# Kernel tuning notes

Hardware: AMD Instinct MI355X
Metric: run time of the kernel (lower is better)

Reference implementation:

```python
import jax, jax.numpy as jnp
import numpy as np

NUM_EMBEDDINGS = 8192
EMBEDDING_DIM = 256
BETA = 0.25


def setup_inputs() -> dict:
    key = jax.random.key(0)
    k1, k2 = jax.random.split(key)
    z = jax.random.normal(k1, (16, 256, 32, 32), dtype=jnp.float32)
    # torch init: uniform(-1/K, 1/K)
    emb_w = jax.random.uniform(k2, (NUM_EMBEDDINGS, EMBEDDING_DIM),
                               dtype=jnp.float32,
                               minval=-1.0 / NUM_EMBEDDINGS,
                               maxval=1.0 / NUM_EMBEDDINGS)
    return {"z": z, "emb_w": emb_w}


def reference(z, emb_w):
    B, C, H, W = z.shape
    z_bhwc = jnp.transpose(z, (0, 2, 3, 1))          # [B,H,W,C]
    flat = z_bhwc.reshape(-1, C)                      # [N,C]
    d = (jnp.sum(flat * flat, axis=1, keepdims=True)
         + jnp.sum(emb_w * emb_w, axis=1)
         - 2.0 * flat @ emb_w.T)                      # [N,K]
    idx = jnp.argmin(d, axis=1)                       # [N]
    # direct gather (mathematically identical to one-hot @ emb_w)
    quantized = emb_w[idx].reshape(z_bhwc.shape)      # [B,H,W,C]
    q_latent_loss = jnp.mean((jax.lax.stop_gradient(quantized) - z_bhwc) ** 2)
    e_latent_loss = jnp.mean((quantized - jax.lax.stop_gradient(z_bhwc)) ** 2)
    loss = q_latent_loss + BETA * e_latent_loss
    # straight-through estimator
    quantized_st = z_bhwc + jax.lax.stop_gradient(quantized - z_bhwc)
    out = jnp.transpose(quantized_st, (0, 3, 1, 2))   # [B,C,H,W]
    return out, loss, idx.reshape(B, -1)
```

## Files before the change

### kernel.cpp

```cpp
#include <hip/hip_runtime.h>
#include <cstdint>
#include <cstddef>

#define N_PIX   16384
#define K_EMB   8192
#define DDIM    256

#define WS_A8       0
#define WS_E8       4194304
#define WS_KEYS     6291456
#define WS_ZSQ      23068672
#define WS_ESQ      23134208
#define WS_LOSS     23166976
#define WS_CNT      23166984

typedef float f32x4 __attribute__((ext_vector_type(4)));

__device__ __forceinline__ unsigned int f32_sortable(float f) {
    unsigned int u = __float_as_uint(f);
    return (u & 0x80000000u) ? ~u : (u | 0x80000000u);
}

__device__ __forceinline__ unsigned char f2fp8(float x) {
    unsigned ub = __float_as_uint(x);
    unsigned sgn = (ub >> 24) & 0x80u;
    unsigned b = ub & 0x7FFFFFFFu;
    unsigned out;
    if (__uint_as_float(b) < 0.015625f) {
        out = (unsigned)(int)rintf(__uint_as_float(b) * 512.0f);
    } else {
        unsigned r = b + 0x7FFFFu + ((b >> 20) & 1u);
        int er = (int)(r >> 23) - 127;
        out = (unsigned)(((er + 7) << 3) | ((r >> 20) & 7u));
    }
    return (unsigned char)(out | sgn);
}

#if defined(__has_builtin)
#if __has_builtin(__builtin_amdgcn_cvt_pk_fp8_f32)
#define HAVE_CVT_FP8 1
#endif
#endif

__device__ __forceinline__ unsigned pack4_fp8(float a, float b, float c, float d) {
#ifdef HAVE_CVT_FP8
    int pk = 0;
    pk = __builtin_amdgcn_cvt_pk_fp8_f32(a, b, pk, false);
    pk = __builtin_amdgcn_cvt_pk_fp8_f32(c, d, pk, true);
    return (unsigned)pk;
#else
    return (unsigned)f2fp8(a) | ((unsigned)f2fp8(b) << 8)
         | ((unsigned)f2fp8(c) << 16) | ((unsigned)f2fp8(d) << 24);
#endif
}

__device__ __forceinline__ void async16(const unsigned char* g, unsigned char* l) {
    __builtin_amdgcn_global_load_lds(
        (const __attribute__((address_space(1))) void*)g,
        (__attribute__((address_space(3))) void*)l, 16, 0, 0);
}

__device__ __forceinline__ float np_pairwise_sq256(const float* row) {
    float r[16];
#pragma unroll
    for (int j = 0; j < 16; ++j) r[j] = 0.f;
#pragma unroll
    for (int c = 0; c < 256; ++c) {
        float x  = row[c];
        float sq = __fmul_rn(x, x);
        int slot = ((c >> 7) << 3) | (c & 7);
        r[slot] = __fadd_rn(r[slot], sq);
    }
    float h0 = __fadd_rn(
        __fadd_rn(__fadd_rn(r[0], r[1]), __fadd_rn(r[2], r[3])),
        __fadd_rn(__fadd_rn(r[4], r[5]), __fadd_rn(r[6], r[7])));
    float h1 = __fadd_rn(
        __fadd_rn(__fadd_rn(r[8], r[9]), __fadd_rn(r[10], r[11])),
        __fadd_rn(__fadd_rn(r[12], r[13]), __fadd_rn(r[14], r[15])));
    return __fadd_rn(h0, h1);
}

__device__ __forceinline__ size_t cm_addr(int r, int c) {
    int ks = c >> 5;
    int h  = (c >> 4) & 1;
    int s  = h ^ ((r >> 2) & 1);
    return (size_t)ks * 4096 + (size_t)r * 32 + s * 16 + (c & 15);
}

__global__ __launch_bounds__(256) void prep_kernel(
        const float* __restrict__ z, const float* __restrict__ emb,
        unsigned char* __restrict__ Af8, unsigned char* __restrict__ Ef8,
        float* __restrict__ zsq, float* __restrict__ esq,
        double* __restrict__ lossAcc, unsigned* __restrict__ doneCnt) {
    __shared__ float tile[32][257];
    int blk = blockIdx.x;
    int t   = threadIdx.x;
    if (blk < 512) {
        int b   = blk >> 5;
        int hw0 = (blk & 31) * 32;
        const float* zb = z + (size_t)b * 262144 + hw0;
        int px = t & 31;
        int cb = t >> 5;
#pragma unroll
        for (int cc = 0; cc < 32; ++cc) {
            int c = cc * 8 + cb;
            tile[px][c] = zb[(size_t)c * 1024 + px];
        }
        __syncthreads();
        int p0 = b * 1024 + hw0;
        int wv = t >> 6, lane = t & 63;
#pragma unroll
        for (int iter = 0; iter < 8; ++iter) {
            int pl = iter * 4 + wv;
            unsigned pk = pack4_fp8(tile[pl][lane * 4 + 0], tile[pl][lane * 4 + 1],
                                    tile[pl][lane * 4 + 2], tile[pl][lane * 4 + 3]);
            int p  = p0 + pl;
            int mb = p >> 7, r = p & 127;
            *(unsigned*)(Af8 + (size_t)mb * 32768 + cm_addr(r, lane * 4)) = pk;
        }
        if (t < 32) zsq[p0 + t] = np_pairwise_sq256(tile[t]);
        if (blk == 0 && t == 0) { *lossAcc = 0.0; *doneCnt = 0u; }
    } else {
        int k0 = (blk - 512) * 32;
        const float4* eg = (const float4*)(emb + (size_t)k0 * DDIM);
#pragma unroll
        for (int i = 0; i < 8; ++i) {
            int idx = i * 256 + t;
            int row = idx >> 6, c4 = idx & 63;
            float4 v = eg[idx];
            *(float4*)&tile[row][c4 * 4] = v;
        }
        __syncthreads();
#pragma unroll
        for (int i = 0; i < 8; ++i) {
            int idx = i * 256 + t;
            int row = idx >> 6, c4 = idx & 63;
            const float* rp = &tile[row][c4 * 4];
            int kg = k0 + row;
            int nb = kg >> 7, rr = kg & 127;
            *(unsigned*)(Ef8 + (size_t)nb * 32768 + cm_addr(rr, c4 * 4)) =
                pack4_fp8(rp[0] * 8192.0f, rp[1] * 8192.0f,
                          rp[2] * 8192.0f, rp[3] * 8192.0f);
        }
        if (t < 32) esq[k0 + t] = np_pairwise_sq256(tile[t]);
    }
}

__device__ __forceinline__ unsigned pack_key(float w) {
    float uf = __builtin_fmaf(w, -512.0f, 262144.0f);
    uf = fminf(uf, 524287.0f);
    unsigned u = (unsigned)uf;
    return (u << 13) | (__float_as_uint(w) & 0x1FFFu);
}

__global__ __launch_bounds__(256) void mfma_score_kernel(
        const unsigned char* __restrict__ Af8,
        const unsigned char* __restrict__ Ef8,
        unsigned int* __restrict__ keys) {
    union SM {
        struct { unsigned char As[8][4096]; unsigned char Bs[8][4096]; } k;
        struct { uint2 ep[128][33]; } e;
    };
    __shared__ SM sm;

    const int g  = blockIdx.x;
    const int mb = blockIdx.y;
    const int t = threadIdx.x;
    const int w = t >> 6, lane = t & 63;
    const int wm = w >> 1, wn = w & 1;
    const int quad = lane >> 4, l16 = lane & 15;

    const unsigned char* Ag = Af8 + (size_t)mb * 32768 + t * 16;
#pragma unroll
    for (int ks = 0; ks < 8; ++ks)
        async16(Ag + ks * 4096, &sm.k.As[ks][t * 16]);
    {
        const unsigned char* Eg = Ef8 + (size_t)(g * 4) * 32768 + t * 16;
#pragma unroll
        for (int ks = 0; ks < 8; ++ks)
            async16(Eg + ks * 4096, &sm.k.Bs[ks][t * 16]);
    }

    int aaddr[4], baddr[4];
#pragma unroll
    for (int fi = 0; fi < 4; ++fi) {
        int row = wm * 64 + fi * 16 + l16;
        int gg  = (quad >> 1) ^ ((row >> 2) & 1);
        aaddr[fi] = row * 32 + gg * 16 + (quad & 1) * 8;
    }
#pragma unroll
    for (int fj = 0; fj < 4; ++fj) {
        int row = wn * 64 + fj * 16 + l16;
        int gg  = (quad >> 1) ^ ((row >> 2) & 1);
        baddr[fj] = row * 32 + gg * 16 + (quad & 1) * 8;
    }

    __syncthreads();

    long long afr[4][8];
#pragma unroll
    for (int fi = 0; fi < 4; ++fi)
#pragma unroll
        for (int ks = 0; ks < 8; ++ks)
            afr[fi][ks] = *(const long long*)&sm.k.As[ks][aaddr[fi]];

    const float NEGINF = __int_as_float(0xFF800000);
    float t2a[16], t2b[16];
#pragma unroll
    for (int i = 0; i < 16; ++i) { t2a[i] = NEGINF; t2b[i] = NEGINF; }

#pragma unroll 1
    for (int j = 0; j < 4; ++j) {
        f32x4 acc[4][4];
#pragma unroll
        for (int i = 0; i < 4; ++i)
#pragma unroll
            for (int jj = 0; jj < 4; ++jj)
#pragma unroll
                for (int r = 0; r < 4; ++r) acc[i][jj][r] = 0.f;

#pragma unroll
        for (int ks = 0; ks < 8; ++ks) {
            long long bfr[4];
#pragma unroll
            for (int fj = 0; fj < 4; ++fj)
                bfr[fj] = *(const long long*)&sm.k.Bs[ks][baddr[fj]];
            __builtin_amdgcn_s_setprio(1);
#pragma unroll
            for (int fi = 0; fi < 4; ++fi)
#pragma unroll
                for (int fj = 0; fj < 4; ++fj)
                    acc[fi][fj] = __builtin_amdgcn_mfma_f32_16x16x32_fp8_fp8(
                        afr[fi][ks], bfr[fj], acc[fi][fj], 0, 0, 0);
            __builtin_amdgcn_s_setprio(0);
        }
        __syncthreads();

        if (j < 3) {
            const unsigned char* Eg =
                Ef8 + (size_t)(g * 4 + j + 1) * 32768 + t * 16;
#pragma unroll
            for (int ks = 0; ks < 8; ++ks)
                async16(Eg + ks * 4096, &sm.k.Bs[ks][t * 16]);
        }

        const int nb = g * 4 + j;
        const unsigned idx0 = (unsigned)(nb * 128 + wn * 64 + l16);
#pragma unroll
        for (int fi = 0; fi < 4; ++fi) {
#pragma unroll
            for (int r = 0; r < 4; ++r) {
                const int ai = fi * 4 + r;
                float a0 = t2a[ai], b0 = t2b[ai];
#pragma unroll
                for (int fj = 0; fj < 4; ++fj) {
                    float v = acc[fi][fj][r];
                    float wv = __uint_as_float(
                        (__float_as_uint(v) & 0xFFFFE000u) | (idx0 + fj * 16));
                    float mn = fminf(a0, wv);
                    a0 = fmaxf(a0, wv);
                    b0 = fmaxf(b0, mn);
                }
                t2a[ai] = a0; t2b[ai] = b0;
            }
        }
        __syncthreads();
    }

#pragma unroll
    for (int fi = 0; fi < 4; ++fi) {
#pragma unroll
        for (int r = 0; r < 4; ++r) {
            const int ai = fi * 4 + r;
            int row = wm * 64 + fi * 16 + quad * 4 + r;
            sm.e.ep[row][wn * 16 + l16] =
                make_uint2(pack_key(t2a[ai]), pack_key(t2b[ai]));
        }
    }
    __syncthreads();

    {
        int row = t >> 1, half = t & 1, h0 = half * 16;
        uint2 mv = sm.e.ep[row][h0];
#pragma unroll
        for (int i = 1; i < 16; ++i) {
            uint2 av = sm.e.ep[row][h0 + i];
            unsigned n0 = min(mv.x, av.x);
            unsigned n1 = min(max(mv.x, av.x), min(mv.y, av.y));
            mv.x = n0; mv.y = n1;
        }
        ((uint2*)keys)[(size_t)(g * 2 + half) * N_PIX + (mb * 128 + row)] = mv;
    }
}

__global__ __launch_bounds__(256) void final_kernel(
        const unsigned int* __restrict__ keys,
        const float* __restrict__ z, const float* __restrict__ emb,
        const float* __restrict__ zsq, const float* __restrict__ esq,
        float* __restrict__ out, float* __restrict__ idx_out,
        float* __restrict__ loss_out,
        double* __restrict__ lossAcc, unsigned* __restrict__ doneCnt) {
    __shared__ float ztile[16][260];
    __shared__ uint2 kt[16][33];
    __shared__ int sidx[16];
    int blk = blockIdx.x;
    int b = blk >> 6, hh = blk & 63;
    int t = threadIdx.x;
    int p0 = b * 1024 + hh * 16;
    const float* zb = z + (size_t)b * 262144 + hh * 16;
    {
        int px = t & 15, cb = t >> 4;
#pragma unroll
        for (int cc = 0; cc < 16; ++cc) {
            int c = cc * 16 + cb;
            ztile[px][c] = zb[(size_t)c * 1024 + px];
        }
    }
    {
        const uint2* kg = (const uint2*)keys;
#pragma unroll
        for (int itr = 0; itr < 2; ++itr) {
            int idx = itr * 256 + t;
            int px = idx & 15, hf = idx >> 4;
            kt[px][hf] = kg[(size_t)hf * N_PIX + p0 + px];
        }
    }
    __syncthreads();

    int wq = t >> 6, lane = t & 63;
#pragma unroll 1
    for (int i = 0; i < 4; ++i) {
        int px = wq * 4 + i;
        int p  = p0 + px;
        uint2 ka = (lane < 32) ? kt[px][lane] : make_uint2(~0u, ~0u);
        unsigned m = min(ka.x, ka.y);
#pragma unroll
        for (int off = 32; off >= 1; off >>= 1)
            m = min(m, (unsigned)__shfl_xor((int)m, off, 64));
        unsigned thr = (m >> 13) + 1600;

        float4 zv = *(const float4*)&ztile[px][lane * 4];
        float zs = zsq[p];
        unsigned long long best = ~0ull;
#pragma unroll 1
        for (int pass = 0; pass < 2; ++pass) {
            unsigned kv = (pass == 0) ? ka.x : ka.y;
            unsigned long long mm = __ballot((kv >> 13) <= thr);
            while (mm) {
                int src = (int)__builtin_ctzll(mm);
                mm &= mm - 1;
                unsigned keyv = (unsigned)__shfl((int)kv, src, 64);
                int k = (int)(keyv & 0x1FFFu);
                const float4 ev = *(const float4*)(emb + (size_t)k * DDIM + lane * 4);
                double d = (double)zv.x * ev.x + (double)zv.y * ev.y
                         + (double)zv.z * ev.z + (double)zv.w * ev.w;
#pragma unroll
                for (int off = 32; off >= 1; off >>= 1)
                    d += __shfl_down(d, off, 64);
                d = __shfl(d, 0, 64);
                float df = (float)d;
                float s  = __fsub_rn(__fadd_rn(zs, esq[k]), __fmul_rn(2.0f, df));
                unsigned long long key =
                    ((unsigned long long)f32_sortable(s) << 32) | (unsigned)k;
                best = key < best ? key : best;
            }
        }
        if (lane == 0) {
            int k = (int)(unsigned)(best & 0xffffffffu);
            sidx[px] = k;
            idx_out[p] = (float)k;
        }
    }
    __syncthreads();

    int px2 = t & 15, cy = t >> 4;
    int kk = sidx[px2];
    const float* er = emb + (size_t)kk * DDIM;
    float* ob = out + (size_t)b * 262144 + hh * 16;
    float local = 0.f;
#pragma unroll 4
    for (int it = 0; it < 16; ++it) {
        int c = it * 16 + cy;
        float q = er[c];
        float d = q - ztile[px2][c];
        ob[(size_t)c * 1024 + px2] = q;
        local += d * d;
    }
#pragma unroll
    for (int off = 32; off >= 1; off >>= 1) local += __shfl_down(local, off, 64);
    __shared__ float wsum[4];
    if ((t & 63) == 0) wsum[t >> 6] = local;
    __syncthreads();
    if (t == 0) {
        double s = (double)wsum[0] + (double)wsum[1]
                 + (double)wsum[2] + (double)wsum[3];
        atomicAdd(lossAcc, s);
        __threadfence();
        unsigned old = atomicAdd(doneCnt, 1u);
        if (old == 1023u) {
            double tot = atomicAdd(lossAcc, 0.0);
            *loss_out = (float)(tot * (1.25 / 4194304.0));
        }
    }
}

extern "C" void kernel_launch(void* const* d_in, const int* in_sizes, int n_in,
                              void* d_out, int out_size, void* d_ws, size_t ws_size,
                              hipStream_t stream) {
    const float* z   = (const float*)d_in[0];
    const float* emb = (const float*)d_in[1];
    float* out = (float*)d_out;
    char* ws = (char*)d_ws;

    unsigned char* Af8 = (unsigned char*)(ws + WS_A8);
    unsigned char* Ef8 = (unsigned char*)(ws + WS_E8);
    unsigned int* keys = (unsigned int*)(ws + WS_KEYS);
    float* zsq      = (float*)(ws + WS_ZSQ);
    float* esq      = (float*)(ws + WS_ESQ);
    double* lossAcc = (double*)(ws + WS_LOSS);
    unsigned* doneCnt = (unsigned*)(ws + WS_CNT);

    prep_kernel<<<768, 256, 0, stream>>>(z, emb, Af8, Ef8, zsq, esq,
                                         lossAcc, doneCnt);
    mfma_score_kernel<<<dim3(16, 128), 256, 0, stream>>>(Af8, Ef8, keys);
    final_kernel<<<1024, 256, 0, stream>>>(keys, z, emb, zsq, esq,
                                           out, out + 4194305, out + 4194304,
                                           lossAcc, doneCnt);
}
```

Before: 197.9 us.

## Compact rerank candidates into shared list and score them with 16-lane groups

The final kernel's exact-distance rerank is restructured. Candidate codes for each of the 16 pixels are first compacted into shared memory with a prefix-sum offset table. They are then scored in double precision by 16-lane groups over a flat candidate list, and the best key per pixel is found by a grouped min reduction. Previously one wave processed each candidate serially with a 64-lane shuffle reduction. This is meant to balance uneven candidate counts across waves and shorten reductions, at the cost of extra shared memory, barriers and a binary search per candidate. The prep kernel's z tile load also now uses float4 global reads.

```diff
diff --git a/kernel.cpp b/kernel.cpp
--- a/kernel.cpp
+++ b/kernel.cpp
@@ -99,12 +99,16 @@
         int b   = blk >> 5;
         int hw0 = (blk & 31) * 32;
         const float* zb = z + (size_t)b * 262144 + hw0;
-        int px = t & 31;
-        int cb = t >> 5;
-#pragma unroll
-        for (int cc = 0; cc < 32; ++cc) {
-            int c = cc * 8 + cb;
-            tile[px][c] = zb[(size_t)c * 1024 + px];
+        int c0  = t >> 3;
+        int px4 = t & 7;
+#pragma unroll
+        for (int cc = 0; cc < 8; ++cc) {
+            int c = cc * 32 + c0;
+            float4 v = *(const float4*)&zb[(size_t)c * 1024 + px4 * 4];
+            tile[px4 * 4 + 0][c] = v.x;
+            tile[px4 * 4 + 1][c] = v.y;
+            tile[px4 * 4 + 2][c] = v.z;
+            tile[px4 * 4 + 3][c] = v.w;
         }
         __syncthreads();
         int p0 = b * 1024 + hw0;
@@ -302,7 +306,14 @@
         double* __restrict__ lossAcc, unsigned* __restrict__ doneCnt) {
     __shared__ float ztile[16][260];
     __shared__ uint2 kt[16][33];
-    __shared__ int sidx[16];
+    __shared__ int   scand[16][64];
+    __shared__ unsigned long long ckey[1024];
+    __shared__ int   soff[17];
+    __shared__ int   scnt[16];
+    __shared__ int   pxmap[1024];
+    __shared__ float szs[16];
+    __shared__ int   sidx[16];
+
     int blk = blockIdx.x;
     int b = blk >> 6, hh = blk & 63;
     int t = threadIdx.x;
@@ -325,50 +336,102 @@
             kt[px][hf] = kg[(size_t)hf * N_PIX + p0 + px];
         }
     }
-    __syncthreads();
-
-    int wq = t >> 6, lane = t & 63;
+    if (t < 16) szs[t] = zsq[p0 + t];
+    __syncthreads();
+
+    {
+        int wq = t >> 6, lane = t & 63;
 #pragma unroll 1
-    for (int i = 0; i < 4; ++i) {
-        int px = wq * 4 + i;
-        int p  = p0 + px;
-        uint2 ka = (lane < 32) ? kt[px][lane] : make_uint2(~0u, ~0u);
-        unsigned m = min(ka.x, ka.y);
-#pragma unroll
-        for (int off = 32; off >= 1; off >>= 1)
-            m = min(m, (unsigned)__shfl_xor((int)m, off, 64));
-        unsigned thr = (m >> 13) + 1600;
-
-        float4 zv = *(const float4*)&ztile[px][lane * 4];
-        float zs = zsq[p];
+        for (int i = 0; i < 4; ++i) {
+            int px = wq * 4 + i;
+            uint2 ka = (lane < 32) ? kt[px][lane] : make_uint2(~0u, ~0u);
+            unsigned m = min(ka.x, ka.y);
+#pragma unroll
+            for (int off = 32; off >= 1; off >>= 1)
+                m = min(m, (unsigned)__shfl_xor((int)m, off, 64));
+            unsigned thr = (m >> 13) + 1600;
+
+            bool h0 = (lane < 32) && ((ka.x >> 13) <= thr);
+            bool h1 = (lane < 32) && ((ka.y >> 13) <= thr);
+            unsigned long long m0 = __ballot(h0);
+            unsigned long long m1 = __ballot(h1);
+            int c0 = __popcll(m0);
+            unsigned long long below = (lane == 63) ? ~0ull >> 1
+                                     : ((1ull << lane) - 1);
+            if (h0) scand[px][__popcll(m0 & below)] = (int)(ka.x & 0x1FFFu);
+            if (h1) scand[px][c0 + __popcll(m1 & below)] = (int)(ka.y & 0x1FFFu);
+            if (lane == 0) scnt[px] = c0 + __popcll(m1);
+        }
+    }
+    __syncthreads();
+
+    if (t < 64) {
+        int v = (t < 16) ? scnt[t] : 0;
+#pragma unroll
+        for (int o = 1; o < 16; o <<= 1) {
+            int u = __shfl_up(v, o, 64);
+            if (t >= o) v += u;
+        }
+        if (t < 16) soff[t + 1] = v;
+        if (t == 0) soff[0] = 0;
+    }
+    __syncthreads();
+    int total = soff[16];
+    for (int f = t; f < total; f += 256) {
+        int lo = 0, hi = 15;
+        while (lo < hi) {
+            int mid = (lo + hi + 1) >> 1;
+            if (soff[mid] <= f) lo = mid; else hi = mid - 1;
+        }
+        pxmap[f] = lo;
+    }
+    __syncthreads();
+
+    {
+        int gid = t >> 4, l16 = t & 15;
+        const float4* emb4 = (const float4*)emb;
+#pragma unroll 1
+        for (int f = gid; f < total; f += 16) {
+            int px = pxmap[f];
+            int k  = scand[px][f - soff[px]];
+            double d = 0.0;
+#pragma unroll
+            for (int q = 0; q < 4; ++q) {
+                float4 ev = emb4[(size_t)k * 64 + q * 16 + l16];
+                const float* zp = &ztile[px][(q * 16 + l16) * 4];
+                d += (double)zp[0] * ev.x + (double)zp[1] * ev.y
+                   + (double)zp[2] * ev.z + (double)zp[3] * ev.w;
+            }
+#pragma unroll
+            for (int o = 1; o < 16; o <<= 1) d += __shfl_xor(d, o, 64);
+            if (l16 == 0) {
+                float df = (float)d;
+                float s  = __fsub_rn(__fadd_rn(szs[px], esq[k]),
+                                     __fmul_rn(2.0f, df));
+                ckey[f] = ((unsigned long long)f32_sortable(s) << 32)
+                        | (unsigned)k;
+            }
+        }
+    }
+    __syncthreads();
+
+    {
+        int cpx = t >> 4, ci = t & 15;
         unsigned long long best = ~0ull;
-#pragma unroll 1
-        for (int pass = 0; pass < 2; ++pass) {
-            unsigned kv = (pass == 0) ? ka.x : ka.y;
-            unsigned long long mm = __ballot((kv >> 13) <= thr);
-            while (mm) {
-                int src = (int)__builtin_ctzll(mm);
-                mm &= mm - 1;
-                unsigned keyv = (unsigned)__shfl((int)kv, src, 64);
-                int k = (int)(keyv & 0x1FFFu);
-                const float4 ev = *(const float4*)(emb + (size_t)k * DDIM + lane * 4);
-                double d = (double)zv.x * ev.x + (double)zv.y * ev.y
-                         + (double)zv.z * ev.z + (double)zv.w * ev.w;
-#pragma unroll
-                for (int off = 32; off >= 1; off >>= 1)
-                    d += __shfl_down(d, off, 64);
-                d = __shfl(d, 0, 64);
-                float df = (float)d;
-                float s  = __fsub_rn(__fadd_rn(zs, esq[k]), __fmul_rn(2.0f, df));
-                unsigned long long key =
-                    ((unsigned long long)f32_sortable(s) << 32) | (unsigned)k;
-                best = key < best ? key : best;
-            }
-        }
-        if (lane == 0) {
+        for (int f = soff[cpx] + ci; f < soff[cpx + 1]; f += 16) {
+            unsigned long long v = ckey[f];
+            best = v < best ? v : best;
+        }
+#pragma unroll
+        for (int o = 1; o < 16; o <<= 1) {
+            unsigned long long ov =
+                (unsigned long long)__shfl_xor((long long)best, o, 64);
+            best = ov < best ? ov : best;
+        }
+        if (ci == 0) {
             int k = (int)(unsigned)(best & 0xffffffffu);
-            sidx[px] = k;
-            idx_out[p] = (float)k;
+            sidx[cpx] = k;
+            idx_out[p0 + cpx] = (float)k;
         }
     }
     __syncthreads();
```

Result: faster. 189.1 us (-4.4%).
